# Performance work log

Hardware: AMD Instinct MI355X
Metric: run time of the kernel (lower is better)

## Reference

```python
import jax, jax.numpy as jnp
import numpy as np

N_NODES = 50000
N_EDGES = 800000
NFEAT, NHID, NCLASS = 512, 128, 64


def setup_inputs() -> dict:
    key = jax.random.key(0)
    ks = jax.random.split(key, 8)
    rows = jnp.sort(jax.random.randint(ks[1], (N_EDGES,), 0, N_NODES, dtype=jnp.int64 if jax.config.jax_enable_x64 else jnp.int32))
    cols = jax.random.randint(ks[2], (N_EDGES,), 0, N_NODES, dtype=rows.dtype)
    return {
        "x": jax.random.normal(ks[0], (N_NODES, NFEAT), dtype=jnp.float32),
        "rows": rows,
        "cols": cols,
        "vals": jax.random.uniform(ks[3], (N_EDGES,), dtype=jnp.float32),
        "W1": jax.random.normal(ks[4], (NFEAT, NHID), dtype=jnp.float32) * (1.0 / np.sqrt(NHID)),
        "b1": jax.random.normal(ks[5], (NHID,), dtype=jnp.float32) * 0.01,
        "W2": jax.random.normal(ks[6], (NHID, NCLASS), dtype=jnp.float32) * (1.0 / np.sqrt(NCLASS)),
        "b2": jax.random.normal(ks[7], (NCLASS,), dtype=jnp.float32) * 0.01,
    }


def _spmm(rows, cols, vals, h, num_nodes):
    # A @ h where A is sparse (num_nodes x num_nodes) given as COO edges.
    # Equivalent math to the custom flexspmm segmented SpMM kernel.
    msgs = vals[:, None] * h[cols]              # [E, d]
    return jax.ops.segment_sum(msgs, rows, num_segments=num_nodes)


def reference(x, rows, cols, vals, W1, b1, W2, b2):
    n = x.shape[0]
    # Layer 1: A @ (X W1) + b1   (GraphConvolution)
    h = x @ W1
    h = _spmm(rows, cols, vals, h, n) + b1
    h = jax.nn.relu(h)
    # dropout: eval mode -> identity
    # Layer 2: (A @ h) W2 + b2   (GraphConvolution2)
    h = _spmm(rows, cols, vals, h, n)
    logits = h @ W2 + b2
    return jax.nn.log_softmax(logits, axis=1)
```

## Files before the change

kernel.cpp:

```cpp
#include <hip/hip_runtime.h>
#include <hip/hip_bf16.h>
#include <math.h>


#define N_NODES 50000
#define N_EDGES 800000
#define NFEAT   512
#define NHID    128
#define NCLASS  64

typedef short  short8  __attribute__((ext_vector_type(8)));
typedef unsigned short ushort8 __attribute__((ext_vector_type(8)));
typedef float  f32x4   __attribute__((ext_vector_type(4)));

static __device__ __forceinline__ float bflo(unsigned int p) {
    return __builtin_bit_cast(float, p << 16);
}
static __device__ __forceinline__ float bfhi(unsigned int p) {
    return __builtin_bit_cast(float, p & 0xFFFF0000u);
}
static __device__ __forceinline__ unsigned short f2bf(float f) {
    unsigned int b = __builtin_bit_cast(unsigned int, f);
    return (unsigned short)((b + 0x7FFFu + ((b >> 16) & 1u)) >> 16);
}
static __device__ __forceinline__ float bf2f(unsigned short u) {
    return __builtin_bit_cast(float, ((unsigned int)u) << 16);
}

__global__ __launch_bounds__(128) void w1t_kernel(
        const float* __restrict__ W1, unsigned short* __restrict__ W1T) {
    const int n = blockIdx.x;
    for (int k = threadIdx.x; k < NFEAT; k += 128)
        W1T[(size_t)n * NFEAT + k] = f2bf(W1[(size_t)k * NHID + n]);
}

__global__ __launch_bounds__(256) void build_rowptr_kernel(
        const int* __restrict__ rows, int* __restrict__ row_ptr) {
    const int e = blockIdx.x * 256 + threadIdx.x;
    if (e >= N_EDGES) return;
    const int re = rows[e];
    if (e == 0) {
        for (int r = 0; r <= re; ++r) row_ptr[r] = 0;
    } else {
        const int rp = rows[e - 1];
        for (int r = rp + 1; r <= re; ++r) row_ptr[r] = e;
    }
    if (e == N_EDGES - 1) {
        for (int r = re + 1; r <= N_NODES; ++r) row_ptr[r] = N_EDGES;
    }
}

__global__ __launch_bounds__(256) void gemm1_kernel(
        const float* __restrict__ x, const unsigned short* __restrict__ W1T,
        unsigned short* __restrict__ h1b, int M) {
    __shared__ unsigned short sA[128 * 64];
    __shared__ unsigned short sB[128 * 64];

    const int tid  = threadIdx.x;
    const int lane = tid & 63;
    const int wid  = tid >> 6;
    const int wr   = wid >> 1, wc = wid & 1;
    const int row0 = blockIdx.x * 128;

    f32x4 acc[4][4];
    #pragma unroll
    for (int i = 0; i < 4; ++i)
        #pragma unroll
        for (int j = 0; j < 4; ++j)
            acc[i][j] = (f32x4){0.f, 0.f, 0.f, 0.f};

    const int srow = tid >> 1;
    const int h    = tid & 1;

    for (int kt = 0; kt < NFEAT; kt += 64) {
        {
            float v[32];
            const float* src = x + (size_t)(row0 + srow) * NFEAT + kt + h * 32;
            if (row0 + srow < M) {
                #pragma unroll
                for (int i = 0; i < 8; ++i)
                    *(float4*)&v[i * 4] = *(const float4*)(src + i * 4);
            } else {
                #pragma unroll
                for (int i = 0; i < 32; ++i) v[i] = 0.f;
            }
            #pragma unroll
            for (int i = 0; i < 4; ++i) {
                ushort8 w;
                #pragma unroll
                for (int q = 0; q < 8; ++q) w[q] = f2bf(v[i * 8 + q]);
                const int gran = (h * 4 + i) ^ (srow & 7);
                *(ushort8*)((char*)sA + srow * 128 + gran * 16) = w;
            }
        }
        {
            const unsigned short* srcb = W1T + (size_t)srow * NFEAT + kt + h * 32;
            #pragma unroll
            for (int i = 0; i < 4; ++i) {
                ushort8 w = *(const ushort8*)(srcb + i * 8);
                const int gran = (h * 4 + i) ^ (srow & 7);
                *(ushort8*)((char*)sB + srow * 128 + gran * 16) = w;
            }
        }
        __syncthreads();

        #pragma unroll
        for (int ks = 0; ks < 2; ++ks) {
            short8 af[4], bfr[4];
            #pragma unroll
            for (int f = 0; f < 4; ++f) {
                const int ar = wr * 64 + f * 16 + (lane & 15);
                const int ag = (ks * 4 + (lane >> 4)) ^ (ar & 7);
                af[f] = *(const short8*)((const char*)sA + ar * 128 + ag * 16);
                const int br = wc * 64 + f * 16 + (lane & 15);
                const int bg = (ks * 4 + (lane >> 4)) ^ (br & 7);
                bfr[f] = *(const short8*)((const char*)sB + br * 128 + bg * 16);
            }
            #pragma unroll
            for (int i = 0; i < 4; ++i)
                #pragma unroll
                for (int j = 0; j < 4; ++j)
                    acc[i][j] = __builtin_amdgcn_mfma_f32_16x16x32_bf16(
                        af[i], bfr[j], acc[i][j], 0, 0, 0);
        }
        __syncthreads();
    }

    const int cr = (lane >> 4) * 4;
    const int cc = lane & 15;
    #pragma unroll
    for (int i = 0; i < 4; ++i)
        #pragma unroll
        for (int j = 0; j < 4; ++j)
            #pragma unroll
            for (int reg = 0; reg < 4; ++reg) {
                const int row = row0 + wr * 64 + i * 16 + cr + reg;
                const int col = wc * 64 + j * 16 + cc;
                if (row < M)
                    h1b[(size_t)row * NHID + col] = f2bf(acc[i][j][reg]);
            }
}

__global__ __launch_bounds__(64) void spmm1_kernel(
        const int* __restrict__ row_ptr, const int* __restrict__ cols,
        const float* __restrict__ vals, const unsigned short* __restrict__ h1b,
        const float* __restrict__ b1, unsigned short* __restrict__ h2b) {
    const int r = blockIdx.x;
    const int j = threadIdx.x;
    const int lo = row_ptr[r];
    const int hi = row_ptr[r + 1];

    float a0 = 0.f, a1 = 0.f;
    int e = lo;
    for (; e + 4 <= hi; e += 4) {
        int   c0 = cols[e],     c1 = cols[e + 1], c2 = cols[e + 2], c3 = cols[e + 3];
        float v0 = vals[e],     v1 = vals[e + 1], v2 = vals[e + 2], v3 = vals[e + 3];
        unsigned int p0 = *(const unsigned int*)(h1b + (size_t)c0 * NHID + 2 * j);
        unsigned int p1 = *(const unsigned int*)(h1b + (size_t)c1 * NHID + 2 * j);
        unsigned int p2 = *(const unsigned int*)(h1b + (size_t)c2 * NHID + 2 * j);
        unsigned int p3 = *(const unsigned int*)(h1b + (size_t)c3 * NHID + 2 * j);
        a0 = fmaf(v0, bflo(p0), a0); a1 = fmaf(v0, bfhi(p0), a1);
        a0 = fmaf(v1, bflo(p1), a0); a1 = fmaf(v1, bfhi(p1), a1);
        a0 = fmaf(v2, bflo(p2), a0); a1 = fmaf(v2, bfhi(p2), a1);
        a0 = fmaf(v3, bflo(p3), a0); a1 = fmaf(v3, bfhi(p3), a1);
    }
    for (; e < hi; ++e) {
        unsigned int p = *(const unsigned int*)(h1b + (size_t)cols[e] * NHID + 2 * j);
        a0 = fmaf(vals[e], bflo(p), a0);
        a1 = fmaf(vals[e], bfhi(p), a1);
    }

    a0 += b1[2 * j];
    a1 += b1[2 * j + 1];
    a0 = a0 > 0.f ? a0 : 0.f;
    a1 = a1 > 0.f ? a1 : 0.f;
    const unsigned int packed = (unsigned int)f2bf(a0) | ((unsigned int)f2bf(a1) << 16);
    *(unsigned int*)(h2b + (size_t)r * NHID + 2 * j) = packed;
}

__global__ __launch_bounds__(256) void gemm2_kernel(
        const unsigned short* __restrict__ h2b, const float* __restrict__ W2,
        unsigned short* __restrict__ tb, int M) {
    __shared__ float sW[NHID * NCLASS];
    for (int i = threadIdx.x; i < NHID * NCLASS / 4; i += 256)
        ((float4*)sW)[i] = ((const float4*)W2)[i];
    __syncthreads();

    const int wave = threadIdx.x >> 6;
    const int lane = threadIdx.x & 63;
    const int row0 = blockIdx.x * 64 + wave * 16;

    for (int i = 0; i < 16; ++i) {
        const int row = row0 + i;
        if (row >= M) break;
        const ushort8* hr = (const ushort8*)(h2b + (size_t)row * NHID);
        float acc = 0.f;
        #pragma unroll
        for (int k8 = 0; k8 < NHID / 8; ++k8) {
            ushort8 hv = hr[k8];
            #pragma unroll
            for (int q = 0; q < 8; ++q)
                acc = fmaf(bf2f(hv[q]), sW[(k8 * 8 + q) * NCLASS + lane], acc);
        }
        tb[(size_t)row * NCLASS + lane] = f2bf(acc);
    }
}

__global__ __launch_bounds__(64) void spmm2_lsm_kernel(
        const int* __restrict__ row_ptr, const int* __restrict__ cols,
        const float* __restrict__ vals, const unsigned short* __restrict__ tb,
        const float* __restrict__ b2, float* __restrict__ out) {
    const int r = blockIdx.x;
    const int j = threadIdx.x;
    const int lo = row_ptr[r];
    const int hi = row_ptr[r + 1];

    float acc = 0.f;
    int e = lo;
    for (; e + 4 <= hi; e += 4) {
        int   c0 = cols[e],     c1 = cols[e + 1], c2 = cols[e + 2], c3 = cols[e + 3];
        float v0 = vals[e],     v1 = vals[e + 1], v2 = vals[e + 2], v3 = vals[e + 3];
        float g0 = bf2f(tb[(size_t)c0 * NCLASS + j]);
        float g1 = bf2f(tb[(size_t)c1 * NCLASS + j]);
        float g2 = bf2f(tb[(size_t)c2 * NCLASS + j]);
        float g3 = bf2f(tb[(size_t)c3 * NCLASS + j]);
        acc = fmaf(v0, g0, acc);
        acc = fmaf(v1, g1, acc);
        acc = fmaf(v2, g2, acc);
        acc = fmaf(v3, g3, acc);
    }
    for (; e < hi; ++e)
        acc = fmaf(vals[e], bf2f(tb[(size_t)cols[e] * NCLASS + j]), acc);

    const float l = acc + b2[j];

    float m = l;
    #pragma unroll
    for (int off = 32; off > 0; off >>= 1)
        m = fmaxf(m, __shfl_xor(m, off, 64));
    float s = __expf(l - m);
    #pragma unroll
    for (int off = 32; off > 0; off >>= 1)
        s += __shfl_xor(s, off, 64);

    out[(size_t)r * NCLASS + j] = (l - m) - __logf(s);
}

extern "C" void kernel_launch(void* const* d_in, const int* in_sizes, int n_in,
                              void* d_out, int out_size, void* d_ws, size_t ws_size,
                              hipStream_t stream) {
    const float* x    = (const float*)d_in[0];
    const int*   rows = (const int*)  d_in[1];
    const int*   cols = (const int*)  d_in[2];
    const float* vals = (const float*)d_in[3];
    const float* W1   = (const float*)d_in[4];
    const float* b1   = (const float*)d_in[5];
    const float* W2   = (const float*)d_in[6];
    const float* b2   = (const float*)d_in[7];
    float* out = (float*)d_out;

    unsigned short* h1b = (unsigned short*)d_ws;
    unsigned short* h2b = h1b + (size_t)N_NODES * NHID;
    unsigned short* tb  = h2b + (size_t)N_NODES * NHID;
    unsigned short* W1T = tb  + (size_t)N_NODES * NCLASS;
    int* row_ptr = (int*)(W1T + (size_t)NHID * NFEAT);

    const int M = N_NODES;

    w1t_kernel<<<NHID, 128, 0, stream>>>(W1, W1T);
    build_rowptr_kernel<<<(N_EDGES + 255) / 256, 256, 0, stream>>>(rows, row_ptr);
    gemm1_kernel<<<(M + 127) / 128, 256, 0, stream>>>(x, W1T, h1b, M);
    spmm1_kernel<<<M, 64, 0, stream>>>(row_ptr, cols, vals, h1b, b1, h2b);
    gemm2_kernel<<<(M + 63) / 64, 256, 0, stream>>>(h2b, W2, tb, M);
    spmm2_lsm_kernel<<<M, 64, 0, stream>>>(row_ptr, cols, vals, tb, b2, out);
}
```

Measured before the change: 286.8 us.

## Fuse prep kernels, use MFMA for gemm2, persistent-wave SpMM kernels

Merges the W1 transpose and row_ptr build into one prep kernel that also transposes W2 to bf16. gemm1 drops to 64-row tiles so more blocks are launched. gemm2 becomes an MFMA kernel with W2 fragments held in registers. Both SpMM kernels become grid-stride persistent waves with deeper load batching, and spmm2 has each half-wave handle alternate edges on packed bf16 pairs. The intent is fewer launches, better occupancy and more memory-level parallelism, at the cost of more register pressure and static grid sizing.

```diff
diff --git a/kernel.cpp b/kernel.cpp
--- a/kernel.cpp
+++ b/kernel.cpp
@@ -23,101 +23,109 @@
     unsigned int b = __builtin_bit_cast(unsigned int, f);
     return (unsigned short)((b + 0x7FFFu + ((b >> 16) & 1u)) >> 16);
 }
-static __device__ __forceinline__ float bf2f(unsigned short u) {
-    return __builtin_bit_cast(float, ((unsigned int)u) << 16);
-}
-
-__global__ __launch_bounds__(128) void w1t_kernel(
-        const float* __restrict__ W1, unsigned short* __restrict__ W1T) {
-    const int n = blockIdx.x;
-    for (int k = threadIdx.x; k < NFEAT; k += 128)
-        W1T[(size_t)n * NFEAT + k] = f2bf(W1[(size_t)k * NHID + n]);
-}
-
-__global__ __launch_bounds__(256) void build_rowptr_kernel(
-        const int* __restrict__ rows, int* __restrict__ row_ptr) {
-    const int e = blockIdx.x * 256 + threadIdx.x;
-    if (e >= N_EDGES) return;
-    const int re = rows[e];
-    if (e == 0) {
-        for (int r = 0; r <= re; ++r) row_ptr[r] = 0;
-    } else {
-        const int rp = rows[e - 1];
-        for (int r = rp + 1; r <= re; ++r) row_ptr[r] = e;
-    }
-    if (e == N_EDGES - 1) {
-        for (int r = re + 1; r <= N_NODES; ++r) row_ptr[r] = N_EDGES;
+
+__global__ __launch_bounds__(256) void prep_kernel(
+        const float* __restrict__ W1, const float* __restrict__ W2,
+        const int* __restrict__ rows,
+        unsigned short* __restrict__ W1T, unsigned short* __restrict__ W2T,
+        int* __restrict__ row_ptr) {
+    const int tid = blockIdx.x * 256 + threadIdx.x;
+    const int T   = gridDim.x * 256;
+    for (int e = tid; e < N_EDGES; e += T) {
+        const int re = rows[e];
+        if (e == 0) {
+            for (int r = 0; r <= re; ++r) row_ptr[r] = 0;
+        } else {
+            const int rp = rows[e - 1];
+            for (int r = rp + 1; r <= re; ++r) row_ptr[r] = e;
+        }
+        if (e == N_EDGES - 1) {
+            for (int r = re + 1; r <= N_NODES; ++r) row_ptr[r] = N_EDGES;
+        }
+    }
+    for (int i = tid; i < NHID * NFEAT; i += T) {
+        const int n = i >> 9, k = i & 511;
+        W1T[i] = f2bf(W1[(size_t)k * NHID + n]);
+    }
+    for (int i = tid; i < NCLASS * NHID; i += T) {
+        const int n = i >> 7, k = i & 127;
+        W2T[i] = f2bf(W2[(size_t)k * NCLASS + n]);
     }
 }
 
 __global__ __launch_bounds__(256) void gemm1_kernel(
         const float* __restrict__ x, const unsigned short* __restrict__ W1T,
         unsigned short* __restrict__ h1b, int M) {
-    __shared__ unsigned short sA[128 * 64];
+    __shared__ unsigned short sA[64 * 64];
     __shared__ unsigned short sB[128 * 64];
 
     const int tid  = threadIdx.x;
     const int lane = tid & 63;
     const int wid  = tid >> 6;
     const int wr   = wid >> 1, wc = wid & 1;
-    const int row0 = blockIdx.x * 128;
-
-    f32x4 acc[4][4];
+    const int row0 = blockIdx.x * 64;
+
+    f32x4 acc[2][4];
     #pragma unroll
-    for (int i = 0; i < 4; ++i)
+    for (int i = 0; i < 2; ++i)
         #pragma unroll
         for (int j = 0; j < 4; ++j)
             acc[i][j] = (f32x4){0.f, 0.f, 0.f, 0.f};
 
-    const int srow = tid >> 1;
-    const int h    = tid & 1;
+    const int arow = tid >> 2;
+    const int akc  = (tid & 3) * 16;
+    const int bcol = tid >> 1;
+    const int bkh  = (tid & 1) * 32;
 
     for (int kt = 0; kt < NFEAT; kt += 64) {
         {
-            float v[32];
-            const float* src = x + (size_t)(row0 + srow) * NFEAT + kt + h * 32;
-            if (row0 + srow < M) {
+            float v[16];
+            const float* src = x + (size_t)(row0 + arow) * NFEAT + kt + akc;
+            if (row0 + arow < M) {
                 #pragma unroll
-                for (int i = 0; i < 8; ++i)
+                for (int i = 0; i < 4; ++i)
                     *(float4*)&v[i * 4] = *(const float4*)(src + i * 4);
             } else {
                 #pragma unroll
-                for (int i = 0; i < 32; ++i) v[i] = 0.f;
-            }
-            #pragma unroll
-            for (int i = 0; i < 4; ++i) {
+                for (int i = 0; i < 16; ++i) v[i] = 0.f;
+            }
+            #pragma unroll
+            for (int i2 = 0; i2 < 2; ++i2) {
                 ushort8 w;
                 #pragma unroll
-                for (int q = 0; q < 8; ++q) w[q] = f2bf(v[i * 8 + q]);
-                const int gran = (h * 4 + i) ^ (srow & 7);
-                *(ushort8*)((char*)sA + srow * 128 + gran * 16) = w;
+                for (int q = 0; q < 8; ++q) w[q] = f2bf(v[i2 * 8 + q]);
+                const int gran = ((akc >> 3) + i2) ^ (arow & 7);
+                *(ushort8*)((char*)sA + arow * 128 + gran * 16) = w;
             }
         }
         {
-            const unsigned short* srcb = W1T + (size_t)srow * NFEAT + kt + h * 32;
+            const unsigned short* srcb = W1T + (size_t)bcol * NFEAT + kt + bkh;
             #pragma unroll
             for (int i = 0; i < 4; ++i) {
                 ushort8 w = *(const ushort8*)(srcb + i * 8);
-                const int gran = (h * 4 + i) ^ (srow & 7);
-                *(ushort8*)((char*)sB + srow * 128 + gran * 16) = w;
+                const int gran = ((bkh >> 3) + i) ^ (bcol & 7);
+                *(ushort8*)((char*)sB + bcol * 128 + gran * 16) = w;
             }
         }
         __syncthreads();
 
         #pragma unroll
         for (int ks = 0; ks < 2; ++ks) {
-            short8 af[4], bfr[4];
-            #pragma unroll
-            for (int f = 0; f < 4; ++f) {
-                const int ar = wr * 64 + f * 16 + (lane & 15);
-                const int ag = (ks * 4 + (lane >> 4)) ^ (ar & 7);
-                af[f] = *(const short8*)((const char*)sA + ar * 128 + ag * 16);
-                const int br = wc * 64 + f * 16 + (lane & 15);
-                const int bg = (ks * 4 + (lane >> 4)) ^ (br & 7);
-                bfr[f] = *(const short8*)((const char*)sB + br * 128 + bg * 16);
-            }
-            #pragma unroll
-            for (int i = 0; i < 4; ++i)
+            short8 af[2], bfr[4];
+            #pragma unroll
+            for (int i = 0; i < 2; ++i) {
+                const int ar = wr * 32 + i * 16 + (lane & 15);
+                const int gran = (ks * 4 + (lane >> 4)) ^ (ar & 7);
+                af[i] = *(const short8*)((const char*)sA + ar * 128 + gran * 16);
+            }
+            #pragma unroll
+            for (int j = 0; j < 4; ++j) {
+                const int br = wc * 64 + j * 16 + (lane & 15);
+                const int gran = (ks * 4 + (lane >> 4)) ^ (br & 7);
+                bfr[j] = *(const short8*)((const char*)sB + br * 128 + gran * 16);
+            }
+            #pragma unroll
+            for (int i = 0; i < 2; ++i)
                 #pragma unroll
                 for (int j = 0; j < 4; ++j)
                     acc[i][j] = __builtin_amdgcn_mfma_f32_16x16x32_bf16(
@@ -129,121 +137,153 @@
     const int cr = (lane >> 4) * 4;
     const int cc = lane & 15;
     #pragma unroll
-    for (int i = 0; i < 4; ++i)
+    for (int i = 0; i < 2; ++i)
         #pragma unroll
         for (int j = 0; j < 4; ++j)
             #pragma unroll
             for (int reg = 0; reg < 4; ++reg) {
-                const int row = row0 + wr * 64 + i * 16 + cr + reg;
+                const int row = row0 + wr * 32 + i * 16 + cr + reg;
                 const int col = wc * 64 + j * 16 + cc;
                 if (row < M)
                     h1b[(size_t)row * NHID + col] = f2bf(acc[i][j][reg]);
             }
 }
 
-__global__ __launch_bounds__(64) void spmm1_kernel(
+__global__ __launch_bounds__(256) void spmm1_kernel(
         const int* __restrict__ row_ptr, const int* __restrict__ cols,
         const float* __restrict__ vals, const unsigned short* __restrict__ h1b,
-        const float* __restrict__ b1, unsigned short* __restrict__ h2b) {
-    const int r = blockIdx.x;
-    const int j = threadIdx.x;
-    const int lo = row_ptr[r];
-    const int hi = row_ptr[r + 1];
-
-    float a0 = 0.f, a1 = 0.f;
-    int e = lo;
-    for (; e + 4 <= hi; e += 4) {
-        int   c0 = cols[e],     c1 = cols[e + 1], c2 = cols[e + 2], c3 = cols[e + 3];
-        float v0 = vals[e],     v1 = vals[e + 1], v2 = vals[e + 2], v3 = vals[e + 3];
-        unsigned int p0 = *(const unsigned int*)(h1b + (size_t)c0 * NHID + 2 * j);
-        unsigned int p1 = *(const unsigned int*)(h1b + (size_t)c1 * NHID + 2 * j);
-        unsigned int p2 = *(const unsigned int*)(h1b + (size_t)c2 * NHID + 2 * j);
-        unsigned int p3 = *(const unsigned int*)(h1b + (size_t)c3 * NHID + 2 * j);
-        a0 = fmaf(v0, bflo(p0), a0); a1 = fmaf(v0, bfhi(p0), a1);
-        a0 = fmaf(v1, bflo(p1), a0); a1 = fmaf(v1, bfhi(p1), a1);
-        a0 = fmaf(v2, bflo(p2), a0); a1 = fmaf(v2, bfhi(p2), a1);
-        a0 = fmaf(v3, bflo(p3), a0); a1 = fmaf(v3, bfhi(p3), a1);
-    }
-    for (; e < hi; ++e) {
-        unsigned int p = *(const unsigned int*)(h1b + (size_t)cols[e] * NHID + 2 * j);
-        a0 = fmaf(vals[e], bflo(p), a0);
-        a1 = fmaf(vals[e], bfhi(p), a1);
-    }
-
-    a0 += b1[2 * j];
-    a1 += b1[2 * j + 1];
-    a0 = a0 > 0.f ? a0 : 0.f;
-    a1 = a1 > 0.f ? a1 : 0.f;
-    const unsigned int packed = (unsigned int)f2bf(a0) | ((unsigned int)f2bf(a1) << 16);
-    *(unsigned int*)(h2b + (size_t)r * NHID + 2 * j) = packed;
+        const float* __restrict__ b1, unsigned short* __restrict__ h2b,
+        int nwaves) {
+    const int j    = threadIdx.x & 63;
+    const int wave = (blockIdx.x * 256 + threadIdx.x) >> 6;
+    const float bb0 = b1[2 * j], bb1 = b1[2 * j + 1];
+
+    for (int r = wave; r < N_NODES; r += nwaves) {
+        const int lo = row_ptr[r], hi = row_ptr[r + 1];
+        float a0 = 0.f, a1 = 0.f;
+        int e = lo;
+        for (; e + 8 <= hi; e += 8) {
+            unsigned int p[8];
+            float v[8];
+            #pragma unroll
+            for (int q = 0; q < 8; ++q) {
+                const int c = cols[e + q];
+                v[q] = vals[e + q];
+                p[q] = *(const unsigned int*)(h1b + (size_t)c * NHID + 2 * j);
+            }
+            #pragma unroll
+            for (int q = 0; q < 8; ++q) {
+                a0 = fmaf(v[q], bflo(p[q]), a0);
+                a1 = fmaf(v[q], bfhi(p[q]), a1);
+            }
+        }
+        for (; e < hi; ++e) {
+            const float vv = vals[e];
+            unsigned int p = *(const unsigned int*)(h1b + (size_t)cols[e] * NHID + 2 * j);
+            a0 = fmaf(vv, bflo(p), a0);
+            a1 = fmaf(vv, bfhi(p), a1);
+        }
+        a0 += bb0; a1 += bb1;
+        a0 = a0 > 0.f ? a0 : 0.f;
+        a1 = a1 > 0.f ? a1 : 0.f;
+        *(unsigned int*)(h2b + (size_t)r * NHID + 2 * j) =
+            (unsigned int)f2bf(a0) | ((unsigned int)f2bf(a1) << 16);
+    }
 }
 
 __global__ __launch_bounds__(256) void gemm2_kernel(
-        const unsigned short* __restrict__ h2b, const float* __restrict__ W2,
-        unsigned short* __restrict__ tb, int M) {
-    __shared__ float sW[NHID * NCLASS];
-    for (int i = threadIdx.x; i < NHID * NCLASS / 4; i += 256)
-        ((float4*)sW)[i] = ((const float4*)W2)[i];
-    __syncthreads();
-
-    const int wave = threadIdx.x >> 6;
+        const unsigned short* __restrict__ h2b,
+        const unsigned short* __restrict__ W2T,
+        unsigned short* __restrict__ tb, int nwaves) {
     const int lane = threadIdx.x & 63;
-    const int row0 = blockIdx.x * 64 + wave * 16;
-
-    for (int i = 0; i < 16; ++i) {
-        const int row = row0 + i;
-        if (row >= M) break;
-        const ushort8* hr = (const ushort8*)(h2b + (size_t)row * NHID);
-        float acc = 0.f;
-        #pragma unroll
-        for (int k8 = 0; k8 < NHID / 8; ++k8) {
-            ushort8 hv = hr[k8];
-            #pragma unroll
-            for (int q = 0; q < 8; ++q)
-                acc = fmaf(bf2f(hv[q]), sW[(k8 * 8 + q) * NCLASS + lane], acc);
-        }
-        tb[(size_t)row * NCLASS + lane] = f2bf(acc);
-    }
-}
-
-__global__ __launch_bounds__(64) void spmm2_lsm_kernel(
+    const int wave = (blockIdx.x * 256 + threadIdx.x) >> 6;
+    const int l15 = lane & 15, lg = lane >> 4;
+
+    short8 Bf[4][4];
+    #pragma unroll
+    for (int ks = 0; ks < 4; ++ks)
+        #pragma unroll
+        for (int ct = 0; ct < 4; ++ct)
+            Bf[ks][ct] = *(const short8*)(W2T + (size_t)(ct * 16 + l15) * NHID + ks * 32 + lg * 8);
+
+    const int ntiles = N_NODES / 16;
+    for (int t = wave; t < ntiles; t += nwaves) {
+        const int r0 = t * 16;
+        f32x4 acc[4];
+        #pragma unroll
+        for (int ct = 0; ct < 4; ++ct) acc[ct] = (f32x4){0.f, 0.f, 0.f, 0.f};
+        #pragma unroll
+        for (int ks = 0; ks < 4; ++ks) {
+            short8 af = *(const short8*)(h2b + (size_t)(r0 + l15) * NHID + ks * 32 + lg * 8);
+            #pragma unroll
+            for (int ct = 0; ct < 4; ++ct)
+                acc[ct] = __builtin_amdgcn_mfma_f32_16x16x32_bf16(af, Bf[ks][ct], acc[ct], 0, 0, 0);
+        }
+        #pragma unroll
+        for (int ct = 0; ct < 4; ++ct)
+            #pragma unroll
+            for (int reg = 0; reg < 4; ++reg)
+                tb[(size_t)(r0 + lg * 4 + reg) * NCLASS + ct * 16 + l15] = f2bf(acc[ct][reg]);
+    }
+}
+
+__global__ __launch_bounds__(256) void spmm2_lsm_kernel(
         const int* __restrict__ row_ptr, const int* __restrict__ cols,
         const float* __restrict__ vals, const unsigned short* __restrict__ tb,
-        const float* __restrict__ b2, float* __restrict__ out) {
-    const int r = blockIdx.x;
-    const int j = threadIdx.x;
-    const int lo = row_ptr[r];
-    const int hi = row_ptr[r + 1];
-
-    float acc = 0.f;
-    int e = lo;
-    for (; e + 4 <= hi; e += 4) {
-        int   c0 = cols[e],     c1 = cols[e + 1], c2 = cols[e + 2], c3 = cols[e + 3];
-        float v0 = vals[e],     v1 = vals[e + 1], v2 = vals[e + 2], v3 = vals[e + 3];
-        float g0 = bf2f(tb[(size_t)c0 * NCLASS + j]);
-        float g1 = bf2f(tb[(size_t)c1 * NCLASS + j]);
-        float g2 = bf2f(tb[(size_t)c2 * NCLASS + j]);
-        float g3 = bf2f(tb[(size_t)c3 * NCLASS + j]);
-        acc = fmaf(v0, g0, acc);
-        acc = fmaf(v1, g1, acc);
-        acc = fmaf(v2, g2, acc);
-        acc = fmaf(v3, g3, acc);
-    }
-    for (; e < hi; ++e)
-        acc = fmaf(vals[e], bf2f(tb[(size_t)cols[e] * NCLASS + j]), acc);
-
-    const float l = acc + b2[j];
-
-    float m = l;
-    #pragma unroll
-    for (int off = 32; off > 0; off >>= 1)
-        m = fmaxf(m, __shfl_xor(m, off, 64));
-    float s = __expf(l - m);
-    #pragma unroll
-    for (int off = 32; off > 0; off >>= 1)
-        s += __shfl_xor(s, off, 64);
-
-    out[(size_t)r * NCLASS + j] = (l - m) - __logf(s);
+        const float* __restrict__ b2, float* __restrict__ out, int nwaves) {
+    const int lane = threadIdx.x & 63;
+    const int h = lane >> 5, j = lane & 31;
+    const int wave = (blockIdx.x * 256 + threadIdx.x) >> 6;
+    const float bb0 = b2[2 * j], bb1 = b2[2 * j + 1];
+
+    for (int r = wave; r < N_NODES; r += nwaves) {
+        const int lo = row_ptr[r], hi = row_ptr[r + 1];
+        float a0 = 0.f, a1 = 0.f;
+        int e = lo;
+        for (; e + 8 <= hi; e += 8) {
+            #pragma unroll
+            for (int q = 0; q < 4; ++q) {
+                const int ee = e + 2 * q + h;
+                const float vv = vals[ee];
+                unsigned int p = *(const unsigned int*)(tb + (size_t)cols[ee] * NCLASS + 2 * j);
+                a0 = fmaf(vv, bflo(p), a0);
+                a1 = fmaf(vv, bfhi(p), a1);
+            }
+        }
+        for (; e + 2 <= hi; e += 2) {
+            const int ee = e + h;
+            const float vv = vals[ee];
+            unsigned int p = *(const unsigned int*)(tb + (size_t)cols[ee] * NCLASS + 2 * j);
+            a0 = fmaf(vv, bflo(p), a0);
+            a1 = fmaf(vv, bfhi(p), a1);
+        }
+        if (e < hi && h == 0) {
+            const float vv = vals[e];
+            unsigned int p = *(const unsigned int*)(tb + (size_t)cols[e] * NCLASS + 2 * j);
+            a0 = fmaf(vv, bflo(p), a0);
+            a1 = fmaf(vv, bfhi(p), a1);
+        }
+        a0 += __shfl_xor(a0, 32, 64);
+        a1 += __shfl_xor(a1, 32, 64);
+        const float l0 = a0 + bb0, l1 = a1 + bb1;
+
+        float m = fmaxf(l0, l1);
+        #pragma unroll
+        for (int off = 16; off > 0; off >>= 1)
+            m = fmaxf(m, __shfl_xor(m, off, 64));
+        float s = __expf(l0 - m) + __expf(l1 - m);
+        #pragma unroll
+        for (int off = 16; off > 0; off >>= 1)
+            s += __shfl_xor(s, off, 64);
+        const float ls = __logf(s);
+
+        if (h == 0) {
+            float2 o;
+            o.x = (l0 - m) - ls;
+            o.y = (l1 - m) - ls;
+            *(float2*)(out + (size_t)r * NCLASS + 2 * j) = o;
+        }
+    }
 }
 
 extern "C" void kernel_launch(void* const* d_in, const int* in_sizes, int n_in,
@@ -263,14 +303,14 @@
     unsigned short* h2b = h1b + (size_t)N_NODES * NHID;
     unsigned short* tb  = h2b + (size_t)N_NODES * NHID;
     unsigned short* W1T = tb  + (size_t)N_NODES * NCLASS;
-    int* row_ptr = (int*)(W1T + (size_t)NHID * NFEAT);
+    unsigned short* W2T = W1T + (size_t)NHID * NFEAT;
+    int* row_ptr = (int*)(W2T + (size_t)NCLASS * NHID);
 
     const int M = N_NODES;
 
-    w1t_kernel<<<NHID, 128, 0, stream>>>(W1, W1T);
-    build_rowptr_kernel<<<(N_EDGES + 255) / 256, 256, 0, stream>>>(rows, row_ptr);
-    gemm1_kernel<<<(M + 127) / 128, 256, 0, stream>>>(x, W1T, h1b, M);
-    spmm1_kernel<<<M, 64, 0, stream>>>(row_ptr, cols, vals, h1b, b1, h2b);
-    gemm2_kernel<<<(M + 63) / 64, 256, 0, stream>>>(h2b, W2, tb, M);
-    spmm2_lsm_kernel<<<M, 64, 0, stream>>>(row_ptr, cols, vals, tb, b2, out);
-}
+    prep_kernel<<<2048, 256, 0, stream>>>(W1, W2, rows, W1T, W2T, row_ptr);
+    gemm1_kernel<<<(M + 63) / 64, 256, 0, stream>>>(x, W1T, h1b, M);
+    spmm1_kernel<<<1024, 256, 0, stream>>>(row_ptr, cols, vals, h1b, b1, h2b, 1024 * 4);
+    gemm2_kernel<<<782, 256, 0, stream>>>(h2b, W2T, tb, 782 * 4);
+    spmm2_lsm_kernel<<<1024, 256, 0, stream>>>(row_ptr, cols, vals, tb, b2, out, 1024 * 4);
+}
```

After: 295.7 us. +3.1%, slower.
